# Optimization experiments

Hardware: AMD Instinct MI355X
Metric: run time of the kernel (lower is better)

Reference implementation:

```python
import jax, jax.numpy as jnp
import numpy as np

B, D_IN, D_OUT, E, TOP_K = 8192, 1024, 512, 8, 2  # D_OUT here is gate hidden = D_IN//2
OUT_DIM = 1024
LN_EPS = 1e-5


def setup_inputs() -> dict:
    key = jax.random.key(0)
    ks = jax.random.split(key, 5)
    s_in = 1.0 / np.sqrt(D_IN)
    s_h = 1.0 / np.sqrt(D_OUT)
    return {
        "x": jax.random.normal(ks[0], (B, D_IN), jnp.float32),
        "gate_w1": jax.random.normal(ks[1], (D_IN, D_OUT), jnp.float32) * s_in,
        "gate_b1": jnp.zeros((D_OUT,), jnp.float32),
        "gate_w2": jax.random.normal(ks[2], (D_OUT, E), jnp.float32) * s_h,
        "gate_b2": jnp.zeros((E,), jnp.float32),
        "We": jax.random.normal(ks[3], (E, D_IN, OUT_DIM), jnp.float32) * s_in,
        "be": jnp.zeros((E, OUT_DIM), jnp.float32),
        "ln_g": jnp.ones((E, OUT_DIM), jnp.float32),
        "ln_b": jnp.zeros((E, OUT_DIM), jnp.float32),
    }


def reference(x, gate_w1, gate_b1, gate_w2, gate_b2, We, be, ln_g, ln_b):
    # Gating network: Linear -> GELU (exact) -> Linear
    g = jax.nn.gelu(x @ gate_w1 + gate_b1, approximate=False)
    scores = g @ gate_w2 + gate_b2                       # [B, E]
    topk_s, topk_i = jax.lax.top_k(scores, TOP_K)        # [B, K]
    topk_w = jax.nn.softmax(topk_s, axis=-1)             # softmax over the top-k only
    # Scatter top-k weights into dense per-expert weights [B, E]
    rows = jnp.arange(scores.shape[0])[:, None]
    dense_w = jnp.zeros_like(scores).at[rows, topk_i].add(topk_w)
    # All-expert forward (non-selected experts get weight 0): Linear -> LayerNorm -> GELU
    h = jnp.einsum("bi,eio->beo", x, We) + be            # [B, E, O]
    mu = h.mean(axis=-1, keepdims=True)
    var = jnp.mean(jnp.square(h - mu), axis=-1, keepdims=True)
    h = (h - mu) * jax.lax.rsqrt(var + LN_EPS) * ln_g + ln_b
    h = jax.nn.gelu(h, approximate=False)
    # Weighted combine (Dropout is identity in eval mode)
    return jnp.einsum("beo,be->bo", h, dense_w)          # [B, O]
```

## Files before the change

kernel.cpp:

```cpp
#include <hip/hip_runtime.h>
#include <hip/hip_bf16.h>
#include <math.h>

#define B_ROWS 8192
#define D_INK  1024
#define D_H    512
#define N_E    8
#define OUT_D  1024
#define LN_EPS 1e-5f
#define GAP_TAU 3e-3f

typedef _Float16 f16x8 __attribute__((ext_vector_type(8)));
typedef _Float16 f16x4v __attribute__((ext_vector_type(4)));
typedef float    f32x4  __attribute__((ext_vector_type(4)));

#define GLOBAL_AS __attribute__((address_space(1)))
#define LDS_AS    __attribute__((address_space(3)))

__device__ __forceinline__ void async16(const void* gptr, void* lptr) {
  __builtin_amdgcn_global_load_lds((const GLOBAL_AS unsigned int*)gptr,
                                   (LDS_AS unsigned int*)lptr, 16, 0, 0);
}

__device__ __forceinline__ float gelu_exact(float x) {
  return 0.5f * x * (1.0f + erff(x * 0.707106781186547524f));
}
__device__ __forceinline__ float clamp_diag(float v) {
  return fminf(fmaxf(v, -1e15f), 1e15f);
}

__global__ __launch_bounds__(256) void convert_x_kernel(
    const float4* __restrict__ x4, f16x4v* __restrict__ hi4) {
  int i = blockIdx.x * 256 + threadIdx.x;
  float4 v = x4[i];
  f16x4v h;
  h[0] = (_Float16)v.x; h[1] = (_Float16)v.y;
  h[2] = (_Float16)v.z; h[3] = (_Float16)v.w;
  hi4[i] = h;
}

__global__ void transpose_split_kernel(const float* __restrict__ src,
                                       _Float16* __restrict__ hi,
                                       int R, int C) {
  __shared__ float tile[32][33];
  long base = (long)blockIdx.z * R * C;
  int c0 = blockIdx.x * 32, r0 = blockIdx.y * 32;
  int tx = threadIdx.x, ty = threadIdx.y;
#pragma unroll
  for (int i = ty; i < 32; i += 8)
    tile[i][tx] = src[base + (long)(r0 + i) * C + (c0 + tx)];
  __syncthreads();
#pragma unroll
  for (int i = ty; i < 32; i += 8)
    hi[base + (long)(c0 + i) * R + (r0 + tx)] = (_Float16)tile[tx][i];
}


__device__ __forceinline__ void stage8(const char* const (&ap)[4],
                                       const char* const (&bp)[4], long koff,
                                       char* Ab, char* Bb, int wave) {
#pragma unroll
  for (int i = 0; i < 4; ++i) {
    async16(ap[i] + koff, Ab + (i * 256 + wave * 64) * 16);
    async16(bp[i] + koff, Bb + (i * 256 + wave * 64) * 16);
  }
}

__device__ __forceinline__ void tile_compute(const char* Ab, const char* Bb,
                                             int wm, int wn, int cl, int quad,
                                             f32x4 (&acc)[4][4]) {
#pragma unroll
  for (int ks = 0; ks < 2; ++ks) {
    f16x8 ah[4], bh[4];
#pragma unroll
    for (int mi = 0; mi < 4; ++mi) {
      int row = wm * 64 + mi * 16 + cl;
      ah[mi] = *(const f16x8*)(Ab + row * 128 + (((ks * 4 + quad) ^ (cl & 7)) * 16));
    }
#pragma unroll
    for (int ni = 0; ni < 4; ++ni) {
      int row = wn * 64 + ni * 16 + cl;
      bh[ni] = *(const f16x8*)(Bb + row * 128 + (((ks * 4 + quad) ^ (cl & 7)) * 16));
    }
#pragma unroll
    for (int mi = 0; mi < 4; ++mi)
#pragma unroll
      for (int ni = 0; ni < 4; ++ni)
        acc[mi][ni] = __builtin_amdgcn_mfma_f32_16x16x32_f16(ah[mi], bh[ni], acc[mi][ni], 0, 0, 0);
  }
}

__global__ __launch_bounds__(256) void gate_gemm_kernel(
    const _Float16* __restrict__ xh, const _Float16* __restrict__ wh,
    const float* __restrict__ b1, float* __restrict__ g) {
  __shared__ __align__(16) unsigned short Ah[128 * 64];
  __shared__ __align__(16) unsigned short Bh[64 * 64];
  int tid = threadIdx.x, lane = tid & 63, wave = tid >> 6;
  int wm = wave >> 1, wn = wave & 1;
  int n0 = blockIdx.x * 64, m0 = blockIdx.y * 128;

  const char* pah[4]; const char* pbh[2];
#pragma unroll
  for (int i = 0; i < 4; ++i) {
    int f = i * 256 + tid;
    int rowt = f >> 3, slot = f & 7;
    int seg = slot ^ (rowt & 7);
    pah[i] = (const char*)xh + (long)(m0 + rowt) * (D_INK * 2) + seg * 16;
  }
#pragma unroll
  for (int i = 0; i < 2; ++i) {
    int f = i * 256 + tid;
    int rowt = f >> 3, slot = f & 7;
    int seg = slot ^ (rowt & 7);
    pbh[i] = (const char*)wh + (long)(n0 + rowt) * (D_INK * 2) + seg * 16;
  }
  f32x4 acc[4][2];
#pragma unroll
  for (int mi = 0; mi < 4; ++mi)
#pragma unroll
    for (int ni = 0; ni < 2; ++ni) acc[mi][ni] = (f32x4){0.f, 0.f, 0.f, 0.f};

  int cl = lane & 15, quad = lane >> 4;
  for (int k0 = 0; k0 < D_INK; k0 += 64) {
    long koff = (long)k0 * 2;
#pragma unroll
    for (int i = 0; i < 4; ++i)
      async16(pah[i] + koff, (char*)Ah + (i * 256 + wave * 64) * 16);
#pragma unroll
    for (int i = 0; i < 2; ++i)
      async16(pbh[i] + koff, (char*)Bh + (i * 256 + wave * 64) * 16);
    __syncthreads();
#pragma unroll
    for (int ks = 0; ks < 2; ++ks) {
      f16x8 ah[4], bh[2];
#pragma unroll
      for (int mi = 0; mi < 4; ++mi) {
        int row = wm * 64 + mi * 16 + cl;
        ah[mi] = *(const f16x8*)((const char*)Ah + row * 128 +
                                 (((ks * 4 + quad) ^ (cl & 7)) * 16));
      }
#pragma unroll
      for (int ni = 0; ni < 2; ++ni) {
        int row = wn * 32 + ni * 16 + cl;
        bh[ni] = *(const f16x8*)((const char*)Bh + row * 128 +
                                 (((ks * 4 + quad) ^ (cl & 7)) * 16));
      }
#pragma unroll
      for (int mi = 0; mi < 4; ++mi)
#pragma unroll
        for (int ni = 0; ni < 2; ++ni)
          acc[mi][ni] = __builtin_amdgcn_mfma_f32_16x16x32_f16(ah[mi], bh[ni], acc[mi][ni], 0, 0, 0);
    }
    __syncthreads();
  }
#pragma unroll
  for (int mi = 0; mi < 4; ++mi)
#pragma unroll
    for (int r = 0; r < 4; ++r) {
      int row = m0 + wm * 64 + mi * 16 + quad * 4 + r;
#pragma unroll
      for (int ni = 0; ni < 2; ++ni) {
        int col = n0 + wn * 32 + ni * 16 + cl;
        float v = clamp_diag(acc[mi][ni][r] + b1[col]);
        g[(long)row * D_H + col] = gelu_exact(v);
      }
    }
}

__global__ __launch_bounds__(256) void score_kernel(
    const float* __restrict__ g, const float* __restrict__ w2,
    const float* __restrict__ b2, float* __restrict__ scores,
    int* __restrict__ nflag, int* __restrict__ worklist) {
  int tid = threadIdx.x, lane = tid & 63, wave = tid >> 6;
  int b = blockIdx.x * 4 + wave;
  const float* grow = g + (long)b * D_H + lane * 8;
  float4 g0 = *(const float4*)grow;
  float4 g1 = *(const float4*)(grow + 4);
  float gv[8] = {g0.x, g0.y, g0.z, g0.w, g1.x, g1.y, g1.z, g1.w};
  float acc[8];
#pragma unroll
  for (int e = 0; e < 8; ++e) acc[e] = 0.f;
#pragma unroll
  for (int j = 0; j < 8; ++j) {
    const float* wrow = w2 + (lane * 8 + j) * N_E;
#pragma unroll
    for (int e = 0; e < 8; ++e) acc[e] += gv[j] * wrow[e];
  }
#pragma unroll
  for (int off = 32; off >= 1; off >>= 1)
#pragma unroll
    for (int e = 0; e < 8; ++e) acc[e] += __shfl_xor(acc[e], off, 64);
  if (lane == 0) {
    float s[8];
#pragma unroll
    for (int e = 0; e < 8; ++e) { s[e] = acc[e] + b2[e]; scores[b * N_E + e] = s[e]; }
    int i0 = 0;
#pragma unroll
    for (int e = 1; e < 8; ++e) if (s[e] > s[i0]) i0 = e;
    int i1 = (i0 == 0) ? 1 : 0;
#pragma unroll
    for (int e = 0; e < 8; ++e) if (e != i0 && s[e] > s[i1]) i1 = e;
    float s2 = -3e38f;
#pragma unroll
    for (int e = 0; e < 8; ++e) if (e != i0 && e != i1 && s[e] > s2) s2 = s[e];
    if (s[i1] - s2 < GAP_TAU) {
      int idx = atomicAdd(nflag, 1);
      worklist[idx] = b;
    }
  }
}

__global__ __launch_bounds__(256) void fixup_g_kernel(
    const float* __restrict__ x, const float* __restrict__ w1,
    const float* __restrict__ b1, const int* __restrict__ nflag,
    const int* __restrict__ worklist, double* __restrict__ g64) {
  int n = *nflag;
  int total = n * 2;
  for (int t = blockIdx.x; t < total; t += gridDim.x) {
    int w = t >> 1, half = t & 1;
    int row = worklist[w];
    int col = half * 256 + threadIdx.x;
    const float* xr = x + (long)row * D_INK;
    double a0 = 0.0, a1 = 0.0, a2 = 0.0, a3 = 0.0;
    for (int k = 0; k < D_INK; k += 4) {
      a0 += (double)xr[k + 0] * (double)w1[(long)(k + 0) * D_H + col];
      a1 += (double)xr[k + 1] * (double)w1[(long)(k + 1) * D_H + col];
      a2 += (double)xr[k + 2] * (double)w1[(long)(k + 2) * D_H + col];
      a3 += (double)xr[k + 3] * (double)w1[(long)(k + 3) * D_H + col];
    }
    double s = ((a0 + a1) + (a2 + a3)) + (double)b1[col];
    g64[(long)w * D_H + col] = 0.5 * s * (1.0 + erf(s * 0.70710678118654752440));
  }
}

__global__ __launch_bounds__(256) void fixup_score_kernel(
    const double* __restrict__ g64, const float* __restrict__ w2,
    const float* __restrict__ b2, const int* __restrict__ nflag,
    const int* __restrict__ worklist, float* __restrict__ scores) {
  __shared__ double p2[256];
  int n = *nflag;
  int tid = threadIdx.x;
  for (int w = blockIdx.x; w < n; w += gridDim.x) {
    int row = worklist[w];
    int e = tid & 7, seg = tid >> 3;
    double s = 0.0;
#pragma unroll
    for (int q = seg * 16; q < seg * 16 + 16; ++q)
      s += g64[(long)w * D_H + q] * (double)w2[q * N_E + e];
    p2[tid] = s;
    __syncthreads();
    if (tid < N_E) {
      double t = 0.0;
      for (int i = 0; i < 32; ++i) t += p2[i * 8 + tid];
      scores[row * N_E + tid] = (float)(t + (double)b2[tid]);
    }
    __syncthreads();
  }
}

__global__ __launch_bounds__(256) void select_kernel(
    const float* __restrict__ scores, int* __restrict__ counts,
    int* __restrict__ bucket, float* __restrict__ pair_w,
    int* __restrict__ pair_e) {
  __shared__ int lcnt[N_E];
  __shared__ int lbase[N_E];
  int tid = threadIdx.x;
  int b = blockIdx.x * 256 + tid;
  if (tid < N_E) lcnt[tid] = 0;
  __syncthreads();
  float s[8];
#pragma unroll
  for (int e = 0; e < 8; ++e) s[e] = scores[b * N_E + e];
  int i0 = 0;
#pragma unroll
  for (int e = 1; e < 8; ++e) if (s[e] > s[i0]) i0 = e;
  int i1 = (i0 == 0) ? 1 : 0;
#pragma unroll
  for (int e = 0; e < 8; ++e) if (e != i0 && s[e] > s[i1]) i1 = e;
  float z = expf(s[i1] - s[i0]);
  float inv = 1.0f / (1.0f + z);
  int r0 = atomicAdd(&lcnt[i0], 1);
  int r1 = atomicAdd(&lcnt[i1], 1);
  __syncthreads();
  if (tid < N_E) lbase[tid] = atomicAdd(&counts[tid], lcnt[tid]);
  __syncthreads();
  int p0 = 2 * b, p1 = 2 * b + 1;
  pair_e[p0] = i0; pair_w[p0] = inv;
  pair_e[p1] = i1; pair_w[p1] = z * inv;
  bucket[i0 * B_ROWS + lbase[i0] + r0] = p0;
  bucket[i1 * B_ROWS + lbase[i1] + r1] = p1;
}

__global__ __launch_bounds__(256) void expert_gemm_kernel(
    const _Float16* __restrict__ xh, const _Float16* __restrict__ wet,
    const int* __restrict__ counts, const int* __restrict__ bucket,
    __bf16* __restrict__ h) {
  int nt = blockIdx.x, mt = blockIdx.y, e = blockIdx.z;
  int cnt = counts[e];
  if (mt * 128 >= cnt) return;
  __shared__ __align__(16) unsigned short As[128 * 64];
  __shared__ __align__(16) unsigned short Bs[128 * 64];
  __shared__ int dest_s[128];
  int tid = threadIdx.x, lane = tid & 63, wave = tid >> 6;
  int wm = wave >> 1, wn = wave & 1;
  int n0 = nt * 128;
  if (tid < 128) {
    int idx = mt * 128 + tid;
    dest_s[tid] = (idx < cnt) ? bucket[e * B_ROWS + idx] : 0;
  }
  __syncthreads();
  const char* xb = (const char*)xh;
  const char* wb = (const char*)wet + (long)e * (D_INK * OUT_D * 2);
  const char* aptr[4];
  const char* bptr[4];
#pragma unroll
  for (int i = 0; i < 4; ++i) {
    int f = i * 256 + tid;
    int rowt = f >> 3, slot = f & 7;
    int seg = slot ^ (rowt & 7);
    int rowid = dest_s[rowt] >> 1;
    aptr[i] = xb + (long)rowid * (D_INK * 2) + seg * 16;
    bptr[i] = wb + (long)(n0 + rowt) * (D_INK * 2) + seg * 16;
  }
  f32x4 acc[4][4];
#pragma unroll
  for (int mi = 0; mi < 4; ++mi)
#pragma unroll
    for (int ni = 0; ni < 4; ++ni) acc[mi][ni] = (f32x4){0.f, 0.f, 0.f, 0.f};

  int cl = lane & 15, quad = lane >> 4;
  for (int k0 = 0; k0 < D_INK; k0 += 64) {
    stage8(aptr, bptr, (long)k0 * 2, (char*)As, (char*)Bs, wave);
    __syncthreads();
    tile_compute((const char*)As, (const char*)Bs, wm, wn, cl, quad, acc);
    __syncthreads();
  }
#pragma unroll
  for (int mi = 0; mi < 4; ++mi)
#pragma unroll
    for (int r = 0; r < 4; ++r) {
      int row128 = wm * 64 + mi * 16 + quad * 4 + r;
      if (mt * 128 + row128 < cnt) {
        long dest = dest_s[row128];
        __bf16* hp = h + dest * OUT_D + n0 + wn * 64 + cl;
#pragma unroll
        for (int ni = 0; ni < 4; ++ni)
          hp[ni * 16] = (__bf16)clamp_diag(acc[mi][ni][r]);
      }
    }
}

__global__ __launch_bounds__(256) void ln_combine_kernel(
    const __bf16* __restrict__ h, const float* __restrict__ pair_w,
    const int* __restrict__ pair_e, const float* __restrict__ be,
    const float* __restrict__ ln_g, const float* __restrict__ ln_b,
    float* __restrict__ out) {
  int b = blockIdx.x, tid = threadIdx.x;
  int lane = tid & 63, wave = tid >> 6;
  int c0 = tid * 4;
  __shared__ float red[4][4];
  float hv[2][4];
  float stats[4];
  int ei[2]; float wi[2];
#pragma unroll
  for (int k = 0; k < 2; ++k) {
    int p = 2 * b + k;
    ei[k] = pair_e[p]; wi[k] = pair_w[p];
    const unsigned short* hp = (const unsigned short*)(h + (long)p * OUT_D) + c0;
    ushort4 raw = *(const ushort4*)hp;
    float4 bev = *(const float4*)(be + ei[k] * OUT_D + c0);
    float v0 = __uint_as_float((unsigned)raw.x << 16) + bev.x;
    float v1 = __uint_as_float((unsigned)raw.y << 16) + bev.y;
    float v2 = __uint_as_float((unsigned)raw.z << 16) + bev.z;
    float v3 = __uint_as_float((unsigned)raw.w << 16) + bev.w;
    hv[k][0] = v0; hv[k][1] = v1; hv[k][2] = v2; hv[k][3] = v3;
    stats[2 * k] = v0 + v1 + v2 + v3;
    stats[2 * k + 1] = v0 * v0 + v1 * v1 + v2 * v2 + v3 * v3;
  }
#pragma unroll
  for (int off = 32; off >= 1; off >>= 1)
#pragma unroll
    for (int i = 0; i < 4; ++i) stats[i] += __shfl_xor(stats[i], off, 64);
  if (lane == 0) {
#pragma unroll
    for (int i = 0; i < 4; ++i) red[wave][i] = stats[i];
  }
  __syncthreads();
  float tot[4] = {0.f, 0.f, 0.f, 0.f};
#pragma unroll
  for (int w = 0; w < 4; ++w)
#pragma unroll
    for (int i = 0; i < 4; ++i) tot[i] += red[w][i];
  float outv[4] = {0.f, 0.f, 0.f, 0.f};
#pragma unroll
  for (int k = 0; k < 2; ++k) {
    float mean = tot[2 * k] * (1.0f / OUT_D);
    float var = tot[2 * k + 1] * (1.0f / OUT_D) - mean * mean;
    float rstd = rsqrtf(fmaxf(var, 0.f) + LN_EPS);
    float4 gp = *(const float4*)(ln_g + ei[k] * OUT_D + c0);
    float4 bp = *(const float4*)(ln_b + ei[k] * OUT_D + c0);
    float t0 = (hv[k][0] - mean) * rstd * gp.x + bp.x;
    float t1 = (hv[k][1] - mean) * rstd * gp.y + bp.y;
    float t2 = (hv[k][2] - mean) * rstd * gp.z + bp.z;
    float t3 = (hv[k][3] - mean) * rstd * gp.w + bp.w;
    outv[0] += wi[k] * gelu_exact(t0);
    outv[1] += wi[k] * gelu_exact(t1);
    outv[2] += wi[k] * gelu_exact(t2);
    outv[3] += wi[k] * gelu_exact(t3);
  }
  float4 o; o.x = outv[0]; o.y = outv[1]; o.z = outv[2]; o.w = outv[3];
  *(float4*)(out + (long)b * OUT_D + c0) = o;
}

extern "C" void kernel_launch(void* const* d_in, const int* in_sizes, int n_in,
                              void* d_out, int out_size, void* d_ws, size_t ws_size,
                              hipStream_t stream) {
  const float* x       = (const float*)d_in[0];
  const float* gate_w1 = (const float*)d_in[1];
  const float* gate_b1 = (const float*)d_in[2];
  const float* gate_w2 = (const float*)d_in[3];
  const float* gate_b2 = (const float*)d_in[4];
  const float* We      = (const float*)d_in[5];
  const float* be      = (const float*)d_in[6];
  const float* ln_g    = (const float*)d_in[7];
  const float* ln_b    = (const float*)d_in[8];
  float* out = (float*)d_out;

  char* ws = (char*)d_ws;
  size_t off = 0;
  _Float16* x16h = (_Float16*)(ws + off); off += (size_t)B_ROWS * D_INK * 2;
  _Float16* w1th = (_Float16*)(ws + off); off += (size_t)D_H * D_INK * 2;
  _Float16* wet  = (_Float16*)(ws + off); off += (size_t)N_E * D_INK * OUT_D * 2;
  float* g       = (float*)(ws + off); off += (size_t)B_ROWS * D_H * 4;
  float* scores  = (float*)(ws + off); off += (size_t)B_ROWS * N_E * 4;
  int* counts    = (int*)(ws + off);   off += 64;
  int* nflag     = counts + 8;
  int* worklist  = (int*)(ws + off);   off += (size_t)B_ROWS * 4;
  int* bucket    = (int*)(ws + off);   off += (size_t)N_E * B_ROWS * 4;
  float* pair_w  = (float*)(ws + off); off += (size_t)2 * B_ROWS * 4;
  int* pair_e    = (int*)(ws + off);   off += (size_t)2 * B_ROWS * 4;
  __bf16* h      = (__bf16*)(ws + off); off += (size_t)2 * B_ROWS * OUT_D * 2;
  double* g64    = (double*)h;

  hipMemsetAsync(counts, 0, 64, stream);
  convert_x_kernel<<<B_ROWS * D_INK / 4 / 256, 256, 0, stream>>>(
      (const float4*)x, (f16x4v*)x16h);
  transpose_split_kernel<<<dim3(D_H / 32, D_INK / 32, 1), dim3(32, 8), 0, stream>>>(
      gate_w1, w1th, D_INK, D_H);
  transpose_split_kernel<<<dim3(OUT_D / 32, D_INK / 32, N_E), dim3(32, 8), 0, stream>>>(
      We, wet, D_INK, OUT_D);
  gate_gemm_kernel<<<dim3(D_H / 64, B_ROWS / 128), 256, 0, stream>>>(
      x16h, w1th, gate_b1, g);
  score_kernel<<<B_ROWS / 4, 256, 0, stream>>>(
      g, gate_w2, gate_b2, scores, nflag, worklist);
  fixup_g_kernel<<<512, 256, 0, stream>>>(
      x, gate_w1, gate_b1, nflag, worklist, g64);
  fixup_score_kernel<<<128, 256, 0, stream>>>(
      g64, gate_w2, gate_b2, nflag, worklist, scores);
  select_kernel<<<B_ROWS / 256, 256, 0, stream>>>(
      scores, counts, bucket, pair_w, pair_e);
  expert_gemm_kernel<<<dim3(OUT_D / 128, B_ROWS / 128, N_E), 256, 0, stream>>>(
      x16h, wet, counts, bucket, h);
  ln_combine_kernel<<<B_ROWS, 256, 0, stream>>>(
      h, pair_w, pair_e, be, ln_g, ln_b, out);
}
```

Before: 310.8 us.

## Fuse prep kernels and memset into one launch; merge fixup kernels

Combines the x fp16 conversion, the two weight transposes, and the counts memset into a single prep kernel that dispatches on block index, removing three launches and a memset. The two fixup kernels are merged so the fp64 gate activations stay in LDS rather than round-tripping through global memory. Each fixup block now computes all 512 columns serially, so there are fewer parallel blocks per flagged row, which could lengthen the fixup tail when many rows are flagged.

```diff
diff --git a/kernel.cpp b/kernel.cpp
--- a/kernel.cpp
+++ b/kernel.cpp
@@ -29,30 +29,43 @@
   return fminf(fmaxf(v, -1e15f), 1e15f);
 }
 
-__global__ __launch_bounds__(256) void convert_x_kernel(
-    const float4* __restrict__ x4, f16x4v* __restrict__ hi4) {
-  int i = blockIdx.x * 256 + threadIdx.x;
-  float4 v = x4[i];
-  f16x4v h;
-  h[0] = (_Float16)v.x; h[1] = (_Float16)v.y;
-  h[2] = (_Float16)v.z; h[3] = (_Float16)v.w;
-  hi4[i] = h;
-}
-
-__global__ void transpose_split_kernel(const float* __restrict__ src,
-                                       _Float16* __restrict__ hi,
-                                       int R, int C) {
+__global__ __launch_bounds__(256) void prep_kernel(
+    const float* __restrict__ x, f16x4v* __restrict__ x16h4,
+    const float* __restrict__ gate_w1, _Float16* __restrict__ w1th,
+    const float* __restrict__ We, _Float16* __restrict__ wet,
+    int* __restrict__ counts) {
   __shared__ float tile[32][33];
-  long base = (long)blockIdx.z * R * C;
-  int c0 = blockIdx.x * 32, r0 = blockIdx.y * 32;
-  int tx = threadIdx.x, ty = threadIdx.y;
+  int bid = blockIdx.x, tid = threadIdx.x;
+  if (bid < 8192) {
+    if (bid == 0 && tid < 16) counts[tid] = 0;
+    int i = bid * 256 + tid;
+    float4 v = ((const float4*)x)[i];
+    f16x4v h;
+    h[0] = (_Float16)v.x; h[1] = (_Float16)v.y;
+    h[2] = (_Float16)v.z; h[3] = (_Float16)v.w;
+    x16h4[i] = h;
+    return;
+  }
+  const float* src; _Float16* dst; int C; long base; int c0, r0;
+  if (bid < 8192 + 512) {
+    int b2 = bid - 8192;
+    src = gate_w1; dst = w1th; C = D_H; base = 0;
+    c0 = (b2 & 15) * 32; r0 = (b2 >> 4) * 32;
+  } else {
+    int b3 = bid - 8704;
+    src = We; dst = wet; C = OUT_D;
+    int zx = b3 & 31, zy = (b3 >> 5) & 31, zz = b3 >> 10;
+    base = (long)zz * D_INK * OUT_D;
+    c0 = zx * 32; r0 = zy * 32;
+  }
+  int tx = tid & 31, ty = tid >> 5;
 #pragma unroll
   for (int i = ty; i < 32; i += 8)
     tile[i][tx] = src[base + (long)(r0 + i) * C + (c0 + tx)];
   __syncthreads();
 #pragma unroll
   for (int i = ty; i < 32; i += 8)
-    hi[base + (long)(c0 + i) * R + (r0 + tx)] = (_Float16)tile[tx][i];
+    dst[base + (long)(c0 + i) * D_INK + (r0 + tx)] = (_Float16)tile[tx][i];
 }
 
 
@@ -210,43 +223,37 @@
   }
 }
 
-__global__ __launch_bounds__(256) void fixup_g_kernel(
+__global__ __launch_bounds__(256) void fixup_kernel(
     const float* __restrict__ x, const float* __restrict__ w1,
-    const float* __restrict__ b1, const int* __restrict__ nflag,
-    const int* __restrict__ worklist, double* __restrict__ g64) {
-  int n = *nflag;
-  int total = n * 2;
-  for (int t = blockIdx.x; t < total; t += gridDim.x) {
-    int w = t >> 1, half = t & 1;
-    int row = worklist[w];
-    int col = half * 256 + threadIdx.x;
-    const float* xr = x + (long)row * D_INK;
-    double a0 = 0.0, a1 = 0.0, a2 = 0.0, a3 = 0.0;
-    for (int k = 0; k < D_INK; k += 4) {
-      a0 += (double)xr[k + 0] * (double)w1[(long)(k + 0) * D_H + col];
-      a1 += (double)xr[k + 1] * (double)w1[(long)(k + 1) * D_H + col];
-      a2 += (double)xr[k + 2] * (double)w1[(long)(k + 2) * D_H + col];
-      a3 += (double)xr[k + 3] * (double)w1[(long)(k + 3) * D_H + col];
-    }
-    double s = ((a0 + a1) + (a2 + a3)) + (double)b1[col];
-    g64[(long)w * D_H + col] = 0.5 * s * (1.0 + erf(s * 0.70710678118654752440));
-  }
-}
-
-__global__ __launch_bounds__(256) void fixup_score_kernel(
-    const double* __restrict__ g64, const float* __restrict__ w2,
+    const float* __restrict__ b1, const float* __restrict__ w2,
     const float* __restrict__ b2, const int* __restrict__ nflag,
     const int* __restrict__ worklist, float* __restrict__ scores) {
+  __shared__ double gLDS[512];
   __shared__ double p2[256];
   int n = *nflag;
   int tid = threadIdx.x;
   for (int w = blockIdx.x; w < n; w += gridDim.x) {
     int row = worklist[w];
+    const float* xr = x + (long)row * D_INK;
+#pragma unroll
+    for (int half = 0; half < 2; ++half) {
+      int col = half * 256 + tid;
+      double a0 = 0.0, a1 = 0.0, a2 = 0.0, a3 = 0.0;
+      for (int k = 0; k < D_INK; k += 4) {
+        a0 += (double)xr[k + 0] * (double)w1[(long)(k + 0) * D_H + col];
+        a1 += (double)xr[k + 1] * (double)w1[(long)(k + 1) * D_H + col];
+        a2 += (double)xr[k + 2] * (double)w1[(long)(k + 2) * D_H + col];
+        a3 += (double)xr[k + 3] * (double)w1[(long)(k + 3) * D_H + col];
+      }
+      double s = ((a0 + a1) + (a2 + a3)) + (double)b1[col];
+      gLDS[col] = 0.5 * s * (1.0 + erf(s * 0.70710678118654752440));
+    }
+    __syncthreads();
     int e = tid & 7, seg = tid >> 3;
     double s = 0.0;
 #pragma unroll
     for (int q = seg * 16; q < seg * 16 + 16; ++q)
-      s += g64[(long)w * D_H + q] * (double)w2[q * N_E + e];
+      s += gLDS[q] * (double)w2[q * N_E + e];
     p2[tid] = s;
     __syncthreads();
     if (tid < N_E) {
@@ -440,23 +447,15 @@
   float* pair_w  = (float*)(ws + off); off += (size_t)2 * B_ROWS * 4;
   int* pair_e    = (int*)(ws + off);   off += (size_t)2 * B_ROWS * 4;
   __bf16* h      = (__bf16*)(ws + off); off += (size_t)2 * B_ROWS * OUT_D * 2;
-  double* g64    = (double*)h;
-
-  hipMemsetAsync(counts, 0, 64, stream);
-  convert_x_kernel<<<B_ROWS * D_INK / 4 / 256, 256, 0, stream>>>(
-      (const float4*)x, (f16x4v*)x16h);
-  transpose_split_kernel<<<dim3(D_H / 32, D_INK / 32, 1), dim3(32, 8), 0, stream>>>(
-      gate_w1, w1th, D_INK, D_H);
-  transpose_split_kernel<<<dim3(OUT_D / 32, D_INK / 32, N_E), dim3(32, 8), 0, stream>>>(
-      We, wet, D_INK, OUT_D);
+
+  prep_kernel<<<8192 + 512 + 8192, 256, 0, stream>>>(
+      x, (f16x4v*)x16h, gate_w1, w1th, We, wet, counts);
   gate_gemm_kernel<<<dim3(D_H / 64, B_ROWS / 128), 256, 0, stream>>>(
       x16h, w1th, gate_b1, g);
   score_kernel<<<B_ROWS / 4, 256, 0, stream>>>(
       g, gate_w2, gate_b2, scores, nflag, worklist);
-  fixup_g_kernel<<<512, 256, 0, stream>>>(
-      x, gate_w1, gate_b1, nflag, worklist, g64);
-  fixup_score_kernel<<<128, 256, 0, stream>>>(
-      g64, gate_w2, gate_b2, nflag, worklist, scores);
+  fixup_kernel<<<256, 256, 0, stream>>>(
+      x, gate_w1, gate_b1, gate_w2, gate_b2, nflag, worklist, scores);
   select_kernel<<<B_ROWS / 256, 256, 0, stream>>>(
       scores, counts, bucket, pair_w, pair_e);
   expert_gemm_kernel<<<dim3(OUT_D / 128, B_ROWS / 128, N_E), 256, 0, stream>>>(
```

Measured after the change: 506.0 us. 1.63x slower.
